# Kernel optimization log

Hardware: AMD Instinct MI355X
Metric: run time of the kernel (lower is better)

## Reference

```python
import jax, jax.numpy as jnp
import numpy as np

FX, FY, CX, CY = 320.0, 320.0, 320.0, 240.0
N_MEAS, N_MP, N_KF = 2_000_000, 100_000, 2_000


def setup_inputs() -> dict:
    key = jax.random.key(0)
    k1, k2, k3, k4 = jax.random.split(key, 4)
    tMP = jax.random.normal(k1, (N_MP, 3), jnp.float32)
    # poses: near-identity with a +5 z-translation so projective depth stays away from 0
    tKF = jnp.eye(4, dtype=jnp.float32)[None] + 0.05 * jax.random.normal(k2, (N_KF, 4, 4), jnp.float32)
    tKF = tKF.at[:, 2, 3].add(5.0)
    idxMP = jnp.arange(N_MP, dtype=jnp.int32)
    idxKF = jnp.arange(N_KF, dtype=jnp.int32)
    mKF = jax.random.randint(k3, (N_MEAS,), 0, N_KF).astype(jnp.float32)
    mMP = jax.random.randint(k4, (N_MEAS,), 0, N_MP).astype(jnp.float32)
    measurements = jnp.stack([mKF, mMP], axis=1)  # [N, 2] float ids
    return {"measurements": measurements, "tMP": tMP, "tKF": tKF, "idxMP": idxMP, "idxKF": idxKF}


def reference(measurements, tMP, tKF, idxMP, idxKF):
    # ID -> row-index join. Original does an O(N*K)/O(N*M) broadcast equality via
    # torch.where; ids here are sorted unique, so a sorted join (searchsorted)
    # yields identical indices without materializing the N x M compare.
    iKF = jnp.searchsorted(idxKF, measurements[:, 0].astype(jnp.int32))
    iMP = jnp.searchsorted(idxMP, measurements[:, 1].astype(jnp.int32))
    # homogeneous map points: [M, 4]
    tMPhomo = jnp.concatenate([tMP, jnp.ones((tMP.shape[0], 1), tMP.dtype)], axis=1)
    # gather + batched 4x4 pose @ point: [N, 4]
    pts = jnp.einsum('nij,nj->ni', tKF[iKF], tMPhomo[iMP])
    # perspective divide + intrinsics scale
    ptx = pts[:, 0] / pts[:, 2] * FX + CX
    pty = pts[:, 1] / pts[:, 2] * FY + CY
    return jnp.stack([ptx, pty], axis=1)  # [N, 2]
```

## Files before the change

### kernel.cpp

```cpp
#include <hip/hip_runtime.h>
#include <hip/hip_bf16.h>

#define FX 320.0f
#define FY 320.0f
#define CX 320.0f
#define CY 240.0f

__global__ __launch_bounds__(256) void proj_kernel(
    const float4* __restrict__ meas4,
    const float*  __restrict__ tMP,
    const float4* __restrict__ tKF4,
    float4*       __restrict__ out4,
    const float*  __restrict__ meas,
    float*        __restrict__ out,
    int n)
{
    int i = blockIdx.x * blockDim.x + threadIdx.x;
    int base = 2 * i;
    if (base >= n) return;

    if (base + 1 < n) {
        float4 m = meas4[i];

        int kf0 = (int)m.x;
        int mp0 = (int)m.y;
        int kf1 = (int)m.z;
        int mp1 = (int)m.w;

        const float* p0 = tMP + 3 * mp0;
        const float* p1 = tMP + 3 * mp1;
        float x0 = p0[0], y0 = p0[1], z0 = p0[2];
        float x1 = p1[0], y1 = p1[1], z1 = p1[2];

        float4 a0 = tKF4[4 * kf0 + 0];
        float4 a1 = tKF4[4 * kf0 + 1];
        float4 a2 = tKF4[4 * kf0 + 2];
        float4 b0 = tKF4[4 * kf1 + 0];
        float4 b1 = tKF4[4 * kf1 + 1];
        float4 b2 = tKF4[4 * kf1 + 2];

        float px0 = a0.x * x0 + a0.y * y0 + a0.z * z0 + a0.w;
        float py0 = a1.x * x0 + a1.y * y0 + a1.z * z0 + a1.w;
        float pz0 = a2.x * x0 + a2.y * y0 + a2.z * z0 + a2.w;

        float px1 = b0.x * x1 + b0.y * y1 + b0.z * z1 + b0.w;
        float py1 = b1.x * x1 + b1.y * y1 + b1.z * z1 + b1.w;
        float pz1 = b2.x * x1 + b2.y * y1 + b2.z * z1 + b2.w;

        float inv0 = 1.0f / pz0;
        float inv1 = 1.0f / pz1;

        float4 r;
        r.x = px0 * inv0 * FX + CX;
        r.y = py0 * inv0 * FY + CY;
        r.z = px1 * inv1 * FX + CX;
        r.w = py1 * inv1 * FY + CY;
        out4[i] = r;
    } else {
        int kf = (int)meas[2 * base + 0];
        int mp = (int)meas[2 * base + 1];
        const float* p = tMP + 3 * mp;
        float x = p[0], y = p[1], z = p[2];
        float4 a0 = tKF4[4 * kf + 0];
        float4 a1 = tKF4[4 * kf + 1];
        float4 a2 = tKF4[4 * kf + 2];
        float px = a0.x * x + a0.y * y + a0.z * z + a0.w;
        float py = a1.x * x + a1.y * y + a1.z * z + a1.w;
        float pz = a2.x * x + a2.y * y + a2.z * z + a2.w;
        float inv = 1.0f / pz;
        out[2 * base + 0] = px * inv * FX + CX;
        out[2 * base + 1] = py * inv * FY + CY;
    }
}

extern "C" void kernel_launch(void* const* d_in, const int* in_sizes, int n_in,
                              void* d_out, int out_size, void* d_ws, size_t ws_size,
                              hipStream_t stream) {
    const float* meas = (const float*)d_in[0];
    const float* tMP  = (const float*)d_in[1];
    const float* tKF  = (const float*)d_in[2];

    int n = in_sizes[0] / 2;
    int npairs = (n + 1) / 2;

    dim3 block(256);
    dim3 grid((npairs + 255) / 256);

    proj_kernel<<<grid, block, 0, stream>>>(
        (const float4*)meas, tMP, (const float4*)tKF,
        (float4*)d_out, meas, (float*)d_out, n);
}
```

Measured before the change: 94.72 us.

## Cache keyframe poses in LDS and use persistent grid with vectorized point loads

Copies the top three rows of every keyframe pose (2000×48 bytes, about 96KB) into shared memory once per block. It then switches to a persistent grid-stride loop with 256 blocks of 1024 threads, and loads each map point with a single unaligned 4-float load that is clamped at the array end. The goal is to replace random global gathers of pose rows with LDS reads and to cut the number of point-load instructions. In exchange, every block pays the cost of loading the whole pose table, occupancy is limited to one block per CU by the large LDS use, and poses beyond MAX_KF are silently dropped.

```diff
diff --git a/kernel.cpp b/kernel.cpp
--- a/kernel.cpp
+++ b/kernel.cpp
@@ -1,43 +1,62 @@
 #include <hip/hip_runtime.h>
 #include <hip/hip_bf16.h>
 
-#define FX 320.0f
-#define FY 320.0f
-#define CX 320.0f
-#define CY 240.0f
+#define FXK 320.0f
+#define FYK 320.0f
+#define CXK 320.0f
+#define CYK 240.0f
 
-__global__ __launch_bounds__(256) void proj_kernel(
+#define MAX_KF 2048
+
+typedef float float4u __attribute__((ext_vector_type(4), aligned(4)));
+
+__global__ __launch_bounds__(1024, 1) void proj_kernel(
     const float4* __restrict__ meas4,
     const float*  __restrict__ tMP,
     const float4* __restrict__ tKF4,
     float4*       __restrict__ out4,
     const float*  __restrict__ meas,
     float*        __restrict__ out,
-    int n)
+    int n,
+    int nKF,
+    int nMPf)
 {
-    int i = blockIdx.x * blockDim.x + threadIdx.x;
-    int base = 2 * i;
-    if (base >= n) return;
+    __shared__ float4 sPose[MAX_KF * 3];
+    const int tid = threadIdx.x;
+    const int nChunks = nKF * 3;
+    for (int c = tid; c < nChunks; c += blockDim.x) {
+        int pose = c / 3;
+        int row  = c - pose * 3;
+        sPose[c] = tKF4[pose * 4 + row];
+    }
+    __syncthreads();
 
-    if (base + 1 < n) {
+    const int nPairs = n >> 1;
+    const int stride = gridDim.x * blockDim.x;
+    const int last4  = nMPf - 4;
+
+    for (int i = blockIdx.x * blockDim.x + tid; i < nPairs; i += stride) {
         float4 m = meas4[i];
+        int kf0 = (int)m.x, mp0 = (int)m.y;
+        int kf1 = (int)m.z, mp1 = (int)m.w;
 
-        int kf0 = (int)m.x;
-        int mp0 = (int)m.y;
-        int kf1 = (int)m.z;
-        int mp1 = (int)m.w;
+        int o0 = mp0 * 3, o1 = mp1 * 3;
+        int c0 = o0 > last4 ? last4 : o0;
+        int c1 = o1 > last4 ? last4 : o1;
+        float4u q0 = *(const float4u*)(tMP + c0);
+        float4u q1 = *(const float4u*)(tMP + c1);
+        bool s0 = (c0 != o0), s1 = (c1 != o1);
+        float x0 = s0 ? q0.y : q0.x;
+        float y0 = s0 ? q0.z : q0.y;
+        float z0 = s0 ? q0.w : q0.z;
+        float x1 = s1 ? q1.y : q1.x;
+        float y1 = s1 ? q1.z : q1.y;
+        float z1 = s1 ? q1.w : q1.z;
 
-        const float* p0 = tMP + 3 * mp0;
-        const float* p1 = tMP + 3 * mp1;
-        float x0 = p0[0], y0 = p0[1], z0 = p0[2];
-        float x1 = p1[0], y1 = p1[1], z1 = p1[2];
-
-        float4 a0 = tKF4[4 * kf0 + 0];
-        float4 a1 = tKF4[4 * kf0 + 1];
-        float4 a2 = tKF4[4 * kf0 + 2];
-        float4 b0 = tKF4[4 * kf1 + 0];
-        float4 b1 = tKF4[4 * kf1 + 1];
-        float4 b2 = tKF4[4 * kf1 + 2];
+        const float4* P0 = sPose + kf0 * 3;
+        const float4* P1 = sPose + kf1 * 3;
+        float4 a0 = P0[0], a1 = P0[1], a2 = P0[2];
+        float4 b0 = P1[0], b1 = P1[1], b2 = P1[2];
 
         float px0 = a0.x * x0 + a0.y * y0 + a0.z * z0 + a0.w;
         float py0 = a1.x * x0 + a1.y * y0 + a1.z * z0 + a1.w;
@@ -51,25 +70,28 @@
         float inv1 = 1.0f / pz1;
 
         float4 r;
-        r.x = px0 * inv0 * FX + CX;
-        r.y = py0 * inv0 * FY + CY;
-        r.z = px1 * inv1 * FX + CX;
-        r.w = py1 * inv1 * FY + CY;
+        r.x = px0 * inv0 * FXK + CXK;
+        r.y = py0 * inv0 * FYK + CYK;
+        r.z = px1 * inv1 * FXK + CXK;
+        r.w = py1 * inv1 * FYK + CYK;
         out4[i] = r;
-    } else {
-        int kf = (int)meas[2 * base + 0];
-        int mp = (int)meas[2 * base + 1];
-        const float* p = tMP + 3 * mp;
-        float x = p[0], y = p[1], z = p[2];
-        float4 a0 = tKF4[4 * kf + 0];
-        float4 a1 = tKF4[4 * kf + 1];
-        float4 a2 = tKF4[4 * kf + 2];
+    }
+
+    if ((n & 1) && blockIdx.x == 0 && tid == 0) {
+        int j = n - 1;
+        int kf = (int)meas[2 * j + 0];
+        int mp = (int)meas[2 * j + 1];
+        float x = tMP[3 * mp + 0];
+        float y = tMP[3 * mp + 1];
+        float z = tMP[3 * mp + 2];
+        const float4* P = sPose + kf * 3;
+        float4 a0 = P[0], a1 = P[1], a2 = P[2];
         float px = a0.x * x + a0.y * y + a0.z * z + a0.w;
         float py = a1.x * x + a1.y * y + a1.z * z + a1.w;
         float pz = a2.x * x + a2.y * y + a2.z * z + a2.w;
         float inv = 1.0f / pz;
-        out[2 * base + 0] = px * inv * FX + CX;
-        out[2 * base + 1] = py * inv * FY + CY;
+        out[2 * j + 0] = px * inv * FXK + CXK;
+        out[2 * j + 1] = py * inv * FYK + CYK;
     }
 }
 
@@ -80,13 +102,18 @@
     const float* tMP  = (const float*)d_in[1];
     const float* tKF  = (const float*)d_in[2];
 
-    int n = in_sizes[0] / 2;
-    int npairs = (n + 1) / 2;
+    int n    = in_sizes[0] / 2;
+    int nMPf = in_sizes[1];
+    int nKF  = in_sizes[2] / 16;
+    if (nKF > MAX_KF) nKF = MAX_KF;
 
-    dim3 block(256);
-    dim3 grid((npairs + 255) / 256);
+    int nPairs = n >> 1;
+    int threads = 1024;
+    int blocks = (nPairs + threads - 1) / threads;
+    if (blocks > 256) blocks = 256;
+    if (blocks < 1) blocks = 1;
 
-    proj_kernel<<<grid, block, 0, stream>>>(
+    proj_kernel<<<blocks, threads, 0, stream>>>(
         (const float4*)meas, tMP, (const float4*)tKF,
-        (float4*)d_out, meas, (float*)d_out, n);
+        (float4*)d_out, meas, (float*)d_out, n, nKF, nMPf);
 }
```

After: 86.77 us. 8.4% less time.
